# Kernel optimization log

Measured on AMD Instinct MI355X. Metric: run time of the kernel, lower is better.

## Reference

```python
import jax, jax.numpy as jnp
import numpy as np
import math

BLOCK_SIZE = 512

def _block_attention(query, key, value):
    # query/key/value: [B, S, H, D]; block-wise attention with PER-BLOCK softmax
    # and normalizer accumulation, faithful to _ring_attention_single (causal, no dropout).
    B, S, H, D = query.shape
    bs = BLOCK_SIZE
    nb = S // bs
    scale = 1.0 / math.sqrt(D)
    neg = jnp.where(jnp.triu(jnp.ones((bs, bs), dtype=bool), 1), -jnp.inf, 0.0)  # strict-upper causal mask for diagonal block
    outs = []
    for i in range(nb):  # small fixed number of blocks (8)
        qb = query[:, i * bs:(i + 1) * bs]                      # [B, bs, H, D]
        kb = key[:, :(i + 1) * bs]                              # [B, (i+1)*bs, H, D]
        vb = value[:, :(i + 1) * bs].reshape(B, i + 1, bs, H, D)
        s = jnp.einsum('bqhd,bkhd->bhqk', qb, kb) * scale       # [B, H, bs, (i+1)*bs]
        s = s.reshape(B, H, bs, i + 1, bs)
        s = s.at[:, :, :, i, :].add(neg)                        # causal mask on diagonal block j == i
        p = jax.nn.softmax(s, axis=-1)                          # softmax PER kv block (faithful to source)
        o = jnp.einsum('bhqjk,bjkhd->bqhd', p, vb)              # accumulated block outputs
        norm = p.sum(axis=-1).sum(axis=-1)                      # [B, H, bs] accumulated normalizer (== i+1 per row)
        norm = jnp.clip(norm, 1e-6, None).transpose(0, 2, 1)[..., None]  # [B, bs, H, 1]
        outs.append(o / norm)
    return jnp.concatenate(outs, axis=1)  # [B, S, H, D]


def setup_inputs() -> dict:
    key = jax.random.key(0)
    k1, k2, k3 = jax.random.split(key, 3)
    shape = (2, 4096, 16, 128)
    return {
        'query': jax.random.normal(k1, shape, dtype=jnp.float32),
        'key': jax.random.normal(k2, shape, dtype=jnp.float32),
        'value': jax.random.normal(k3, shape, dtype=jnp.float32),
    }


def reference(query, key, value):
    return _block_attention(query, key, value)
```

## Files before the change

kernel.cpp:

```cpp
#include <hip/hip_runtime.h>

typedef short bf16x8 __attribute__((ext_vector_type(8)));
typedef short bf16x4 __attribute__((ext_vector_type(4)));
typedef float f32x4  __attribute__((ext_vector_type(4)));
typedef float f32x16 __attribute__((ext_vector_type(16)));
typedef unsigned int u32;
typedef u32 u32x4 __attribute__((ext_vector_type(4)));

#define SEQ 4096
#define NH  16
#define HD  128

__device__ __forceinline__ short bf16_rne(float x) {
  u32 u = __builtin_bit_cast(u32, x);
  u = (u + 0x7FFFu + ((u >> 16) & 1u)) >> 16;
  return (short)u;
}

typedef __attribute__((address_space(1))) const void as1c_void;
typedef __attribute__((address_space(3))) void as3_void;

#define CVTPK(d, a, b) asm("v_cvt_pk_bf16_f32 %0, %1, %2" : "=v"(d) : "v"(a), "v"(b))
#define PLSWAP(x, y)   asm("v_permlane32_swap_b32 %0, %1" : "+v"(x), "+v"(y))

__global__ __launch_bounds__(256) void prep_k(const float* __restrict__ K,
                                              short* __restrict__ Kp) {
  int idx = blockIdx.x * 256 + threadIdx.x;
  int d4 = idx & 31;
  int s  = (idx >> 5) & 4095;
  int h  = (idx >> 17) & 15;
  int b  = idx >> 21;
  f32x4 v = *(const f32x4*)(K + (((size_t)(b * SEQ + s) * NH + h) << 7) + d4 * 4);
  bf16x4 o;
  o[0] = bf16_rne(v[0]); o[1] = bf16_rne(v[1]);
  o[2] = bf16_rne(v[2]); o[3] = bf16_rne(v[3]);
  int x = (d4 * 4) ^ ((s & 7) << 3);
  *(bf16x4*)(Kp + (((size_t)(b * NH + h) * SEQ + s) << 7) + x) = o;
}

__global__ __launch_bounds__(256) void prep_v(const float* __restrict__ V,
                                              short* __restrict__ Vt) {
  __shared__ short tile[64 * 128];
  int bid = blockIdx.x;
  int sb = bid & 63;
  int h  = (bid >> 6) & 15;
  int b  = bid >> 10;
  int t = threadIdx.x;
  {
    int s = t >> 2;
    int dbase = (t & 3) * 32;
    const float* src = V + (((size_t)(b * SEQ + sb * 64 + s) * NH + h) << 7) + dbase;
    int sw = (s & 7) << 3;
#pragma unroll
    for (int j = 0; j < 8; ++j) {
      f32x4 v = *(const f32x4*)(src + j * 4);
      bf16x4 o;
      o[0] = bf16_rne(v[0]); o[1] = bf16_rne(v[1]);
      o[2] = bf16_rne(v[2]); o[3] = bf16_rne(v[3]);
      int d = dbase + j * 4;
      *(bf16x4*)&tile[s * 128 + (d ^ sw)] = o;
    }
  }
  __syncthreads();
  {
    int w = t >> 6, l = t & 63, g = l >> 4, lq = l & 15;
    int srel = lq * 4;
#pragma unroll
    for (int j = 0; j < 8; ++j) {
      int d = w * 32 + j * 4 + g;
      bf16x4 o;
#pragma unroll
      for (int i = 0; i < 4; ++i) {
        int s = srel + i;
        o[i] = tile[s * 128 + (d ^ ((s & 7) << 3))];
      }
      int sp = srel ^ ((d & 7) << 3);
      *(bf16x4*)(Vt + (((size_t)(b * NH + h) * HD + d) << 12) + sb * 64 + sp) = o;
    }
  }
}

__global__ __launch_bounds__(256, 2) void attn_main(const float* __restrict__ Q,
                                                    const short* __restrict__ Kp,
                                                    const short* __restrict__ Vt,
                                                    float* __restrict__ Out) {
  __shared__ __align__(16) short sK[2][64 * 128];
  __shared__ __align__(16) short sV[2][128 * 64];

  int bid0 = (int)blockIdx.x;
  int bid = (bid0 & 7) * 64 + (bid0 >> 3);
  int p  = bid & 15;
  int h  = (bid >> 4) & 15;
  int b  = bid >> 8;

  int tid = threadIdx.x;
  int l = tid & 63, w = tid >> 6;
  int q5 = l & 31;
  int hi = l >> 5;
  int hi4 = hi * 4, hi8 = hi * 8;
  int cswz = (l & 7) << 4;

  int kcol[8], vcol[4];
#pragma unroll
  for (int i = 0; i < 8; ++i) kcol[i] = (i * 32 + hi * 16) ^ cswz;
#pragma unroll
  for (int ks = 0; ks < 4; ++ks) vcol[ks] = (ks * 32 + hi * 16) ^ cswz;

  const int pat[16] = {0,1,2,3, 8,9,10,11, 16,17,18,19, 24,25,26,27};

  const char* KbB = (const char*)(Kp + ((size_t)(b * NH + h) << 19));
  const char* VbB = (const char*)(Vt + ((size_t)(b * NH + h) << 19));

  const char* kgb[4]; const char* vgb[4]; int ldo[4];
#pragma unroll
  for (int j = 0; j < 4; ++j) {
    int idx = j * 256 + tid;
    kgb[j] = KbB + idx * 16;
    vgb[j] = VbB + (size_t)(idx >> 3) * 8192 + (idx & 7) * 16;
    ldo[j] = idx * 16;
  }

  const float SCL = 0.08838834764831845f * 1.4426950408889634f;

  for (int ts = 0; ts < 2; ++ts) {
    int qt = ts ? p : (31 - p);
    int iblk = qt >> 2;
    int qrow0 = qt * 128 + w * 32;
    int qg = qrow0 + q5;
    int qgrel = (qt & 3) * 128 + w * 32 + q5;
    int nch_w = (qt & 3) * 2 + (w >> 1) + 1;
    int ntot = 8 * iblk + (qt & 3) * 2 + 2;

    bf16x8 qf[8];
    {
      const float* qp = Q + (((size_t)(b * SEQ + qg) * NH + h) << 7);
#pragma unroll
      for (int i = 0; i < 8; ++i) {
        int d0 = i * 16 + hi8;
        f32x4 a = *(const f32x4*)(qp + d0);
        f32x4 c2 = *(const f32x4*)(qp + d0 + 4);
        bf16x8 f;
        f[0] = bf16_rne(a[0] * SCL);  f[1] = bf16_rne(a[1] * SCL);
        f[2] = bf16_rne(a[2] * SCL);  f[3] = bf16_rne(a[3] * SCL);
        f[4] = bf16_rne(c2[0] * SCL); f[5] = bf16_rne(c2[1] * SCL);
        f[6] = bf16_rne(c2[2] * SCL); f[7] = bf16_rne(c2[3] * SCL);
        qf[i] = f;
      }
    }

    f32x16 ot[4], ob[4];
#pragma unroll
    for (int dt = 0; dt < 4; ++dt) {
#pragma unroll
      for (int r = 0; r < 16; ++r) { ot[dt][r] = 0.f; ob[dt][r] = 0.f; }
    }
    float Z = 0.0f;

    __syncthreads();
#pragma unroll
    for (int j = 0; j < 4; ++j) {
      __builtin_amdgcn_global_load_lds((as1c_void*)kgb[j], (as3_void*)((char*)sK[0] + ldo[j]), 16, 0, 0);
      __builtin_amdgcn_global_load_lds((as1c_void*)vgb[j], (as3_void*)((char*)sV[0] + ldo[j]), 16, 0, 0);
    }

#pragma unroll 2
    for (int t = 0; t < ntot; ++t) {
      __syncthreads();

      int bi = (t + 1) & 1;
      const int more = (t + 1 < ntot);
      if (more) {
#pragma unroll
        for (int j = 0; j < 4; ++j)
          __builtin_amdgcn_global_load_lds((as1c_void*)(kgb[j] + (size_t)(t + 1) * 16384),
                                           (as3_void*)((char*)sK[bi] + ldo[j]), 16, 0, 0);
      }

      int jb = t >> 3, c = t & 7;
      const int diag = (jb == iblk);

      if (!(diag && c >= nch_w)) {
        const char* kbuf = (const char*)sK[t & 1];
        const char* vbuf = (const char*)sV[t & 1];
        float csum = 0.0f;

        f32x16 st0, st1;
#pragma unroll
        for (int r = 0; r < 16; ++r) { st0[r] = 0.f; st1[r] = 0.f; }
        int rowb = q5 * 256;
        __builtin_amdgcn_s_setprio(1);
#pragma unroll
        for (int i = 0; i < 8; ++i) {
          bf16x8 kf = *(const bf16x8*)(kbuf + rowb + kcol[i]);
          st0 = __builtin_amdgcn_mfma_f32_32x32x16_bf16(kf, qf[i], st0, 0, 0, 0);
        }
#pragma unroll
        for (int i = 0; i < 8; ++i) {
          bf16x8 kf = *(const bf16x8*)(kbuf + 8192 + rowb + kcol[i]);
          st1 = __builtin_amdgcn_mfma_f32_32x32x16_bf16(kf, qf[i], st1, 0, 0, 0);
        }
        __builtin_amdgcn_s_setprio(0);

        if (more) {
#pragma unroll
          for (int j = 0; j < 4; ++j)
            __builtin_amdgcn_global_load_lds((as1c_void*)(vgb[j] + (size_t)(t + 1) * 128),
                                             (as3_void*)((char*)sV[bi] + ldo[j]), 16, 0, 0);
        }

        if (diag && c == nch_w - 1) {
          int lim0 = qgrel - c * 64;
          int lim1 = lim0 - 32;
#pragma unroll
          for (int r = 0; r < 16; ++r) {
            int pr4 = pat[r] + hi4;
            if (pr4 > lim0) st0[r] = -1e30f;
            if (pr4 > lim1) st1[r] = -1e30f;
          }
        }

        bf16x8 pa0, pa1, pa2, pa3;
        {
          float pr[16];
#pragma unroll
          for (int r = 0; r < 16; ++r) {
            pr[r] = __builtin_amdgcn_exp2f(st0[r]);
            csum += pr[r];
          }
          u32 X0, X1, Y0, Y1, A0, A1, B0, B1;
          CVTPK(X0, pr[0], pr[1]);   CVTPK(X1, pr[2], pr[3]);
          CVTPK(Y0, pr[4], pr[5]);   CVTPK(Y1, pr[6], pr[7]);
          PLSWAP(X0, Y0); PLSWAP(X1, Y1);
          pa0 = __builtin_bit_cast(bf16x8, (u32x4){X0, X1, Y0, Y1});
          CVTPK(A0, pr[8], pr[9]);   CVTPK(A1, pr[10], pr[11]);
          CVTPK(B0, pr[12], pr[13]); CVTPK(B1, pr[14], pr[15]);
          PLSWAP(A0, B0); PLSWAP(A1, B1);
          pa1 = __builtin_bit_cast(bf16x8, (u32x4){A0, A1, B0, B1});
        }
        __builtin_amdgcn_s_setprio(1);
#pragma unroll
        for (int dt = 0; dt < 4; ++dt) {
          bf16x8 vf = *(const bf16x8*)(vbuf + (dt * 32 + q5) * 128 + vcol[0]);
          ob[dt] = __builtin_amdgcn_mfma_f32_32x32x16_bf16(pa0, vf, ob[dt], 0, 0, 0);
        }
#pragma unroll
        for (int dt = 0; dt < 4; ++dt) {
          bf16x8 vf = *(const bf16x8*)(vbuf + (dt * 32 + q5) * 128 + vcol[1]);
          ob[dt] = __builtin_amdgcn_mfma_f32_32x32x16_bf16(pa1, vf, ob[dt], 0, 0, 0);
        }
        __builtin_amdgcn_s_setprio(0);

        {
          float pr[16];
#pragma unroll
          for (int r = 0; r < 16; ++r) {
            pr[r] = __builtin_amdgcn_exp2f(st1[r]);
            csum += pr[r];
          }
          u32 X0, X1, Y0, Y1, A0, A1, B0, B1;
          CVTPK(X0, pr[0], pr[1]);   CVTPK(X1, pr[2], pr[3]);
          CVTPK(Y0, pr[4], pr[5]);   CVTPK(Y1, pr[6], pr[7]);
          PLSWAP(X0, Y0); PLSWAP(X1, Y1);
          pa2 = __builtin_bit_cast(bf16x8, (u32x4){X0, X1, Y0, Y1});
          CVTPK(A0, pr[8], pr[9]);   CVTPK(A1, pr[10], pr[11]);
          CVTPK(B0, pr[12], pr[13]); CVTPK(B1, pr[14], pr[15]);
          PLSWAP(A0, B0); PLSWAP(A1, B1);
          pa3 = __builtin_bit_cast(bf16x8, (u32x4){A0, A1, B0, B1});
        }
        __builtin_amdgcn_s_setprio(1);
#pragma unroll
        for (int dt = 0; dt < 4; ++dt) {
          bf16x8 vf = *(const bf16x8*)(vbuf + (dt * 32 + q5) * 128 + vcol[2]);
          ob[dt] = __builtin_amdgcn_mfma_f32_32x32x16_bf16(pa2, vf, ob[dt], 0, 0, 0);
        }
#pragma unroll
        for (int dt = 0; dt < 4; ++dt) {
          bf16x8 vf = *(const bf16x8*)(vbuf + (dt * 32 + q5) * 128 + vcol[3]);
          ob[dt] = __builtin_amdgcn_mfma_f32_32x32x16_bf16(pa3, vf, ob[dt], 0, 0, 0);
        }
        __builtin_amdgcn_s_setprio(0);

        Z += csum;
      } else if (more) {
#pragma unroll
        for (int j = 0; j < 4; ++j)
          __builtin_amdgcn_global_load_lds((as1c_void*)(vgb[j] + (size_t)(t + 1) * 128),
                                           (as3_void*)((char*)sV[bi] + ldo[j]), 16, 0, 0);
      }

      if ((t & 7) == 7 || t == ntot - 1) {
        float zf = Z + __shfl_xor(Z, 32, 64);
        float rzL = 1.0f / zf;
        float rz[16];
#pragma unroll
        for (int r = 0; r < 16; ++r) rz[r] = __shfl(rzL, pat[r] + hi4, 64);
#pragma unroll
        for (int dt = 0; dt < 4; ++dt) {
#pragma unroll
          for (int r = 0; r < 16; ++r) {
            ot[dt][r] += ob[dt][r] * rz[r];
            ob[dt][r] = 0.f;
          }
        }
        Z = 0.0f;
      }
    }

    float rnorm = 1.0f / (float)(iblk + 1);
#pragma unroll
    for (int dt = 0; dt < 4; ++dt) {
#pragma unroll
      for (int r = 0; r < 16; ++r) {
        int qrow = qrow0 + pat[r] + hi4;
        Out[(((size_t)(b * SEQ + qrow) * NH + h) << 7) + dt * 32 + q5] = ot[dt][r] * rnorm;
      }
    }
  }
}

extern "C" void kernel_launch(void* const* d_in, const int* in_sizes, int n_in,
                              void* d_out, int out_size, void* d_ws, size_t ws_size,
                              hipStream_t stream) {
  const float* Q = (const float*)d_in[0];
  const float* K = (const float*)d_in[1];
  const float* V = (const float*)d_in[2];
  float* out = (float*)d_out;

  short* Kp = (short*)d_ws;
  short* Vt = Kp + (size_t)2 * NH * SEQ * HD;

  prep_k<<<(2 * NH * SEQ * (HD / 4)) / 256, 256, 0, stream>>>(K, Kp);
  prep_v<<<2 * NH * (SEQ / 64), 256, 0, stream>>>(V, Vt);
  attn_main<<<2 * NH * 16, 256, 0, stream>>>(Q, Kp, Vt, out);
}
```

Measured before the change: 205.8 us.

## Read V fragments directly from global memory instead of staging through LDS

The V tile is no longer double-buffered in shared memory. Each lane now loads its bf16x8 V fragments straight from the pre-swizzled global Vt buffer inside the PV MFMA loops. This halves LDS usage, which could allow more occupancy, and removes the V global-to-LDS copies. In exchange, global load latency now sits directly in the MFMA dependency chain with no prefetch, and the V reads are not shared across the block's waves, so L2 and global traffic go up.

```diff
diff --git a/kernel.cpp b/kernel.cpp
--- a/kernel.cpp
+++ b/kernel.cpp
@@ -85,7 +85,6 @@
                                                     const short* __restrict__ Vt,
                                                     float* __restrict__ Out) {
   __shared__ __align__(16) short sK[2][64 * 128];
-  __shared__ __align__(16) short sV[2][128 * 64];
 
   int bid0 = (int)blockIdx.x;
   int bid = (bid0 & 7) * 64 + (bid0 >> 3);
@@ -111,14 +110,17 @@
   const char* KbB = (const char*)(Kp + ((size_t)(b * NH + h) << 19));
   const char* VbB = (const char*)(Vt + ((size_t)(b * NH + h) << 19));
 
-  const char* kgb[4]; const char* vgb[4]; int ldo[4];
+  const char* kgb[4]; int ldo[4];
 #pragma unroll
   for (int j = 0; j < 4; ++j) {
     int idx = j * 256 + tid;
     kgb[j] = KbB + idx * 16;
-    vgb[j] = VbB + (size_t)(idx >> 3) * 8192 + (idx & 7) * 16;
     ldo[j] = idx * 16;
   }
+
+  const char* vrb[4];
+#pragma unroll
+  for (int dt = 0; dt < 4; ++dt) vrb[dt] = VbB + (size_t)(dt * 32 + q5) * 8192;
 
   const float SCL = 0.08838834764831845f * 1.4426950408889634f;
 
@@ -158,18 +160,15 @@
 
     __syncthreads();
 #pragma unroll
-    for (int j = 0; j < 4; ++j) {
+    for (int j = 0; j < 4; ++j)
       __builtin_amdgcn_global_load_lds((as1c_void*)kgb[j], (as3_void*)((char*)sK[0] + ldo[j]), 16, 0, 0);
-      __builtin_amdgcn_global_load_lds((as1c_void*)vgb[j], (as3_void*)((char*)sV[0] + ldo[j]), 16, 0, 0);
-    }
 
 #pragma unroll 2
     for (int t = 0; t < ntot; ++t) {
       __syncthreads();
 
       int bi = (t + 1) & 1;
-      const int more = (t + 1 < ntot);
-      if (more) {
+      if (t + 1 < ntot) {
 #pragma unroll
         for (int j = 0; j < 4; ++j)
           __builtin_amdgcn_global_load_lds((as1c_void*)(kgb[j] + (size_t)(t + 1) * 16384),
@@ -181,7 +180,7 @@
 
       if (!(diag && c >= nch_w)) {
         const char* kbuf = (const char*)sK[t & 1];
-        const char* vbuf = (const char*)sV[t & 1];
+        const int vco = t * 128;
         float csum = 0.0f;
 
         f32x16 st0, st1;
@@ -200,13 +199,6 @@
           st1 = __builtin_amdgcn_mfma_f32_32x32x16_bf16(kf, qf[i], st1, 0, 0, 0);
         }
         __builtin_amdgcn_s_setprio(0);
-
-        if (more) {
-#pragma unroll
-          for (int j = 0; j < 4; ++j)
-            __builtin_amdgcn_global_load_lds((as1c_void*)(vgb[j] + (size_t)(t + 1) * 128),
-                                             (as3_void*)((char*)sV[bi] + ldo[j]), 16, 0, 0);
-        }
 
         if (diag && c == nch_w - 1) {
           int lim0 = qgrel - c * 64;
@@ -240,12 +232,12 @@
         __builtin_amdgcn_s_setprio(1);
 #pragma unroll
         for (int dt = 0; dt < 4; ++dt) {
-          bf16x8 vf = *(const bf16x8*)(vbuf + (dt * 32 + q5) * 128 + vcol[0]);
+          bf16x8 vf = *(const bf16x8*)(vrb[dt] + vco + vcol[0]);
           ob[dt] = __builtin_amdgcn_mfma_f32_32x32x16_bf16(pa0, vf, ob[dt], 0, 0, 0);
         }
 #pragma unroll
         for (int dt = 0; dt < 4; ++dt) {
-          bf16x8 vf = *(const bf16x8*)(vbuf + (dt * 32 + q5) * 128 + vcol[1]);
+          bf16x8 vf = *(const bf16x8*)(vrb[dt] + vco + vcol[1]);
           ob[dt] = __builtin_amdgcn_mfma_f32_32x32x16_bf16(pa1, vf, ob[dt], 0, 0, 0);
         }
         __builtin_amdgcn_s_setprio(0);
@@ -270,22 +262,17 @@
         __builtin_amdgcn_s_setprio(1);
 #pragma unroll
         for (int dt = 0; dt < 4; ++dt) {
-          bf16x8 vf = *(const bf16x8*)(vbuf + (dt * 32 + q5) * 128 + vcol[2]);
+          bf16x8 vf = *(const bf16x8*)(vrb[dt] + vco + vcol[2]);
           ob[dt] = __builtin_amdgcn_mfma_f32_32x32x16_bf16(pa2, vf, ob[dt], 0, 0, 0);
         }
 #pragma unroll
         for (int dt = 0; dt < 4; ++dt) {
-          bf16x8 vf = *(const bf16x8*)(vbuf + (dt * 32 + q5) * 128 + vcol[3]);
+          bf16x8 vf = *(const bf16x8*)(vrb[dt] + vco + vcol[3]);
           ob[dt] = __builtin_amdgcn_mfma_f32_32x32x16_bf16(pa3, vf, ob[dt], 0, 0, 0);
         }
         __builtin_amdgcn_s_setprio(0);
 
         Z += csum;
-      } else if (more) {
-#pragma unroll
-        for (int j = 0; j < 4; ++j)
-          __builtin_amdgcn_global_load_lds((as1c_void*)(vgb[j] + (size_t)(t + 1) * 128),
-                                           (as3_void*)((char*)sV[bi] + ldo[j]), 16, 0, 0);
       }
 
       if ((t & 7) == 7 || t == ntot - 1) {
```

New measurement: 295.0 us. 1.43x slower.
